# Kernel optimization log

Measured on AMD Instinct MI355X. Metric: run time of the kernel, lower is better.

## Reference

```python
import jax, jax.numpy as jnp
import numpy as np

POOL = (2, 2, 2)   # LPPool3d kernel == stride
KH, KW = 3, 3      # unfold kernel
EPS = 1e-6


def setup_inputs() -> dict:
    key = jax.random.key(0)
    k1, k2, k3 = jax.random.split(key, 3)
    x = jax.random.normal(k1, (32, 8, 4, 256, 256), dtype=jnp.float32)
    patch_dim = 8 * (4 // POOL[0]) * KH * KW  # 144
    out_dim = 128
    lin_w = jax.random.normal(k2, (out_dim, patch_dim), dtype=jnp.float32) * (1.0 / np.sqrt(patch_dim))
    lin_b = jax.random.normal(k3, (out_dim,), dtype=jnp.float32) * 0.01
    return {"x": x, "lin_w": lin_w, "lin_b": lin_b}


def reference(x, lin_w, lin_b):
    N, C, D, H, W = x.shape
    kd, kh, kw = POOL
    # LPPool3d with p=2, stride==kernel: (sum of squares in window)^(1/2)
    xr = (x * x).reshape(N, C, D // kd, kd, H // kh, kh, W // kw, kw)
    pooled = jnp.sqrt(xr.sum(axis=(3, 5, 7)))  # (N, C, Dp, Hp, Wp)
    Dp, Hp, Wp = pooled.shape[2], pooled.shape[3], pooled.shape[4]
    # merge depth into channels: permute(0,2,1,3,4).view(N, Dp*C, Hp, Wp)
    merged = pooled.transpose(0, 2, 1, 3, 4).reshape(N, Dp * C, Hp, Wp)
    MC = Dp * C
    Ho, Wo = Hp - KH + 1, Wp - KW + 1
    # im2col matching torch.nn.Unfold ordering: (channel, kh, kw) flattened
    slices = [merged[:, :, i:i + Ho, j:j + Wo] for i in range(KH) for j in range(KW)]
    patches = jnp.stack(slices, axis=2)                 # (N, MC, KH*KW, Ho, Wo)
    patches = patches.reshape(N, MC * KH * KW, Ho * Wo) # (N, patch_dim, L)
    patches = patches.transpose(0, 2, 1)                # (N, L, patch_dim)
    # per-patch linear + CELU (alpha=1)
    proj = jnp.einsum('nlk,ok->nlo', patches, lin_w) + lin_b  # (N, L, out_dim)
    act = jax.nn.celu(proj)
    # aggregate over patches, then L2-normalize with clamped norm
    agg = act.mean(axis=1)                              # (N, out_dim)
    norm = jnp.maximum(jnp.linalg.norm(agg, axis=1, keepdims=True), EPS)
    return agg / norm
```

## Files before the change

### kernel.cpp

```cpp
#include <hip/hip_runtime.h>
#include <math.h>

#define NB   32
#define C    8
#define D    4
#define H    256
#define W    256
#define HP   128
#define WP   128
#define MC   16
#define HO   126
#define WO   126
#define PATCH 144
#define OUTD 128
#define NL   (HO*WO)
#define HOG  6
#define NGRP (HO/HOG)
#define PROWS 9
#define BROW 168

typedef float  f32x4  __attribute__((ext_vector_type(4)));
typedef __bf16 bf16x8 __attribute__((ext_vector_type(8)));

__global__ __launch_bounds__(256, 2)
void fused_kernel(const float* __restrict__ x, const float* __restrict__ lin_w,
                  const float* __restrict__ lin_b, float* __restrict__ accg) {
    __shared__ __align__(16) char smem[PROWS*128*32 + OUTD*BROW*2];
    __bf16* Pl   = (__bf16*)smem;
    __bf16* Blds = (__bf16*)(smem + PROWS*128*32);

    int blk = blockIdx.x;
    int g = blk % NGRP, n = blk / NGRP;
    int ho0 = g * HOG;
    int t = threadIdx.x;
    int wave = t >> 6, lane = t & 63, quad = lane >> 4, l16 = lane & 15;

    {
        int wp = t & 127, dph = t >> 7;
        const float* xn = x + (size_t)n * (C*D*H*W);
#pragma unroll 2
        for (int i = 0; i < 8; i++) {
            int hp = ho0 + i;
            bf16x8 pk;
#pragma unroll
            for (int c = 0; c < 8; c++) {
                const float* xb = xn + ((c*4 + 2*dph) * H + 2*hp) * W + 2*wp;
                float2 a0 = *(const float2*)(xb);
                float2 a1 = *(const float2*)(xb + W);
                float2 a2 = *(const float2*)(xb + H*W);
                float2 a3 = *(const float2*)(xb + H*W + W);
                float s = a0.x*a0.x + a0.y*a0.y + a1.x*a1.x + a1.y*a1.y
                        + a2.x*a2.x + a2.y*a2.y + a3.x*a3.x + a3.y*a3.y;
                pk[c] = (__bf16)sqrtf(s);
            }
            *(bf16x8*)&Pl[(i*128 + wp)*16 + dph*8] = pk;
        }
        bf16x8 z = {};
        *(bf16x8*)&Pl[(8*128 + wp)*16 + dph*8] = z;
    }

    {
        int o = t & 127, kh = t >> 7;
#pragma unroll 4
        for (int kk = 0; kk < 80; kk++) {
            int kn = kh*80 + kk;
            int tap = kn >> 4, mc = kn & 15;
            float v = (tap < 9) ? lin_w[o*PATCH + mc*9 + tap] : 0.f;
            Blds[o*BROW + kn] = (__bf16)v;
        }
    }

    float lb[8];
#pragma unroll
    for (int nt = 0; nt < 8; nt++) lb[nt] = lin_b[nt*16 + l16];

    __syncthreads();

    float srun[8] = {0,0,0,0,0,0,0,0};
    int h8 = (quad & 1) * 8;
    int m0 = wave * 32 + l16;

    for (int hh = 0; hh < HOG; hh++) {
        f32x4 acc[2][8] = {};
#pragma unroll
        for (int ks = 0; ks < 5; ks++) {
            int tap = 2*ks + (quad >> 1);
            int it = (tap * 11) >> 5;
            int jt = tap - it * 3;
            bf16x8 afr[2];
#pragma unroll
            for (int mt = 0; mt < 2; mt++) {
                int m = m0 + mt*16;
                afr[mt] = *(const bf16x8*)&Pl[((hh + it)*128 + m + jt)*16 + h8];
            }
#pragma unroll
            for (int nt = 0; nt < 8; nt++) {
                bf16x8 bfr = *(const bf16x8*)&Blds[(nt*16 + l16)*BROW + ks*32 + quad*8];
                acc[0][nt] = __builtin_amdgcn_mfma_f32_16x16x32_bf16(afr[0], bfr, acc[0][nt], 0, 0, 0);
                acc[1][nt] = __builtin_amdgcn_mfma_f32_16x16x32_bf16(afr[1], bfr, acc[1][nt], 0, 0, 0);
            }
        }
#pragma unroll
        for (int nt = 0; nt < 8; nt++) {
            float s = 0.f;
#pragma unroll
            for (int mt = 0; mt < 2; mt++) {
                int mb = wave*32 + mt*16 + quad*4;
#pragma unroll
                for (int r = 0; r < 4; r++) {
                    float p = acc[mt][nt][r] + lb[nt];
                    float a = (p > 0.f) ? p : (__expf(p) - 1.f);
                    if (mb + r < WO) s += a;
                }
            }
            s += __shfl_xor(s, 16, 64);
            s += __shfl_xor(s, 32, 64);
            srun[nt] += s;
        }
    }

    __syncthreads();
    float* red = (float*)smem;
    if (quad == 0) {
#pragma unroll
        for (int nt = 0; nt < 8; nt++) red[wave*OUTD + nt*16 + l16] = srun[nt];
    }
    __syncthreads();
    if (t < OUTD) {
        float tot = red[t] + red[OUTD+t] + red[2*OUTD+t] + red[3*OUTD+t];
        atomicAdd(&accg[n*OUTD + t], tot);
    }
}

__global__ void finalize_kernel(const float* __restrict__ acc, float* __restrict__ out) {
    int n = blockIdx.x;
    int o = threadIdx.x;
    float a = acc[n * OUTD + o] * (1.0f / (float)NL);
    float s = a * a;
#pragma unroll
    for (int off = 32; off > 0; off >>= 1) s += __shfl_down(s, off, 64);
    __shared__ float partial[2];
    if ((o & 63) == 0) partial[o >> 6] = s;
    __syncthreads();
    float norm = sqrtf(partial[0] + partial[1]);
    norm = fmaxf(norm, 1e-6f);
    out[n * OUTD + o] = a / norm;
}

extern "C" void kernel_launch(void* const* d_in, const int* in_sizes, int n_in,
                              void* d_out, int out_size, void* d_ws, size_t ws_size,
                              hipStream_t stream) {
    const float* x     = (const float*)d_in[0];
    const float* lin_w = (const float*)d_in[1];
    const float* lin_b = (const float*)d_in[2];
    float* out = (float*)d_out;

    float* acc = (float*)d_ws;

    hipMemsetAsync(acc, 0, NB * OUTD * sizeof(float), stream);
    fused_kernel<<<NB * NGRP, 256, 0, stream>>>(x, lin_w, lin_b, acc);
    finalize_kernel<<<NB, OUTD, 0, stream>>>(acc, out);
}
```

Baseline: 432.6 us.

## Split pooling into separate coalesced kernel writing bf16 intermediate before GEMM

```diff
diff --git a/kernel.cpp b/kernel.cpp
--- a/kernel.cpp
+++ b/kernel.cpp
@@ -18,9 +18,134 @@
 #define NGRP (HO/HOG)
 #define PROWS 9
 #define BROW 168
+#define NPOOLB 2048
 
 typedef float  f32x4  __attribute__((ext_vector_type(4)));
 typedef __bf16 bf16x8 __attribute__((ext_vector_type(8)));
+
+__global__ __launch_bounds__(256, 4)
+void pool_kernel(const float* __restrict__ x, __bf16* __restrict__ Pg) {
+    int t = threadIdx.x;
+    int wp2 = t & 63;
+    int dph = (t >> 6) & 1;
+    int g = blockIdx.x*2 + (t >> 7);
+    int hp = g & 127, n = g >> 7;
+
+    const float* xn = x + (size_t)n * (C*D*H*W) + (size_t)(2*dph) * (H*W)
+                        + (2*hp)*W + 4*wp2;
+    bf16x8 pk0, pk1;
+#pragma unroll 2
+    for (int c = 0; c < 8; c++) {
+        const float* xb = xn + (size_t)c * (D*H*W);
+        f32x4 a0 = *(const f32x4*)(xb);
+        f32x4 a1 = *(const f32x4*)(xb + W);
+        f32x4 a2 = *(const f32x4*)(xb + H*W);
+        f32x4 a3 = *(const f32x4*)(xb + H*W + W);
+        float s0 = a0.x*a0.x + a0.y*a0.y + a1.x*a1.x + a1.y*a1.y
+                 + a2.x*a2.x + a2.y*a2.y + a3.x*a3.x + a3.y*a3.y;
+        float s1 = a0.z*a0.z + a0.w*a0.w + a1.z*a1.z + a1.w*a1.w
+                 + a2.z*a2.z + a2.w*a2.w + a3.z*a3.z + a3.w*a3.w;
+        pk0[c] = (__bf16)sqrtf(s0);
+        pk1[c] = (__bf16)sqrtf(s1);
+    }
+    __bf16* pr = Pg + ((size_t)n*HP + hp) * (WP*MC);
+    *(bf16x8*)&pr[(2*wp2    )*16 + dph*8] = pk0;
+    *(bf16x8*)&pr[(2*wp2 + 1)*16 + dph*8] = pk1;
+}
+
+__global__ __launch_bounds__(256, 2)
+void gemm_kernel(const __bf16* __restrict__ Pg, const float* __restrict__ lin_w,
+                 const float* __restrict__ lin_b, float* __restrict__ accg) {
+    __shared__ __align__(16) char smem[PROWS*128*32 + OUTD*BROW*2];
+    __bf16* Pl   = (__bf16*)smem;
+    __bf16* Blds = (__bf16*)(smem + PROWS*128*32);
+
+    int blk = blockIdx.x;
+    int g = blk % NGRP, n = blk / NGRP;
+    int ho0 = g * HOG;
+    int t = threadIdx.x;
+    int wave = t >> 6, lane = t & 63, quad = lane >> 4, l16 = lane & 15;
+
+    {
+        const f32x4* src = (const f32x4*)(Pg + ((size_t)n*HP + ho0) * (WP*MC));
+        f32x4* dst = (f32x4*)Pl;
+#pragma unroll
+        for (int r = 0; r < 8; r++) dst[r*256 + t] = src[r*256 + t];
+        f32x4 z = {};
+        dst[8*256 + t] = z;
+    }
+    {
+        int o = t & 127, kh = t >> 7;
+#pragma unroll 4
+        for (int kk = 0; kk < 80; kk++) {
+            int kn = kh*80 + kk;
+            int tap = kn >> 4, mc = kn & 15;
+            float v = (tap < 9) ? lin_w[o*PATCH + mc*9 + tap] : 0.f;
+            Blds[o*BROW + kn] = (__bf16)v;
+        }
+    }
+
+    float lb[8];
+#pragma unroll
+    for (int nt = 0; nt < 8; nt++) lb[nt] = lin_b[nt*16 + l16];
+
+    __syncthreads();
+
+    float srun[8] = {0,0,0,0,0,0,0,0};
+    int h8 = (quad & 1) * 8;
+    int m0 = wave * 32 + l16;
+
+    for (int hh = 0; hh < HOG; hh++) {
+        f32x4 acc[2][8] = {};
+#pragma unroll
+        for (int ks = 0; ks < 5; ks++) {
+            int tap = 2*ks + (quad >> 1);
+            int it = (tap * 11) >> 5;
+            int jt = tap - it * 3;
+            bf16x8 afr[2];
+#pragma unroll
+            for (int mt = 0; mt < 2; mt++) {
+                int m = m0 + mt*16;
+                afr[mt] = *(const bf16x8*)&Pl[((hh + it)*128 + m + jt)*16 + h8];
+            }
+#pragma unroll
+            for (int nt = 0; nt < 8; nt++) {
+                bf16x8 bfr = *(const bf16x8*)&Blds[(nt*16 + l16)*BROW + ks*32 + quad*8];
+                acc[0][nt] = __builtin_amdgcn_mfma_f32_16x16x32_bf16(afr[0], bfr, acc[0][nt], 0, 0, 0);
+                acc[1][nt] = __builtin_amdgcn_mfma_f32_16x16x32_bf16(afr[1], bfr, acc[1][nt], 0, 0, 0);
+            }
+        }
+#pragma unroll
+        for (int nt = 0; nt < 8; nt++) {
+            float s = 0.f;
+#pragma unroll
+            for (int mt = 0; mt < 2; mt++) {
+                int mb = wave*32 + mt*16 + quad*4;
+#pragma unroll
+                for (int r = 0; r < 4; r++) {
+                    float p = acc[mt][nt][r] + lb[nt];
+                    float a = (p > 0.f) ? p : (__expf(p) - 1.f);
+                    if (mb + r < WO) s += a;
+                }
+            }
+            s += __shfl_xor(s, 16, 64);
+            s += __shfl_xor(s, 32, 64);
+            srun[nt] += s;
+        }
+    }
+
+    __syncthreads();
+    float* red = (float*)smem;
+    if (quad == 0) {
+#pragma unroll
+        for (int nt = 0; nt < 8; nt++) red[wave*OUTD + nt*16 + l16] = srun[nt];
+    }
+    __syncthreads();
+    if (t < OUTD) {
+        float tot = red[t] + red[OUTD+t] + red[2*OUTD+t] + red[3*OUTD+t];
+        atomicAdd(&accg[n*OUTD + t], tot);
+    }
+}
 
 __global__ __launch_bounds__(256, 2)
 void fused_kernel(const float* __restrict__ x, const float* __restrict__ lin_w,
@@ -58,7 +183,6 @@
         bf16x8 z = {};
         *(bf16x8*)&Pl[(8*128 + wp)*16 + dph*8] = z;
     }
-
     {
         int o = t & 127, kh = t >> 7;
 #pragma unroll 4
@@ -156,8 +280,15 @@
     float* out = (float*)d_out;
 
     float* acc = (float*)d_ws;
-
     hipMemsetAsync(acc, 0, NB * OUTD * sizeof(float), stream);
-    fused_kernel<<<NB * NGRP, 256, 0, stream>>>(x, lin_w, lin_b, acc);
+
+    const size_t PG_BYTES = (size_t)NB * HP * WP * MC * sizeof(__bf16);
+    if (ws_size >= 16384 + PG_BYTES) {
+        __bf16* Pg = (__bf16*)((char*)d_ws + 16384);
+        pool_kernel<<<NPOOLB, 256, 0, stream>>>(x, Pg);
+        gemm_kernel<<<NB * NGRP, 256, 0, stream>>>(Pg, lin_w, lin_b, acc);
+    } else {
+        fused_kernel<<<NB * NGRP, 256, 0, stream>>>(x, lin_w, lin_b, acc);
+    }
     finalize_kernel<<<NB, OUTD, 0, stream>>>(acc, out);
 }
```

Result: no change. 429.1 us (-0.8%).
